# Optimization experiments

Hardware: AMD Instinct MI355X
Metric: run time of the kernel (lower is better)

Reference implementation:

```python
import jax, jax.numpy as jnp
import numpy as np

N, E = 100000, 1600000
NF, HC, NC = 32, 64, 64


def setup_inputs() -> dict:
    key = jax.random.key(0)
    ks = jax.random.split(key, 12)
    s = 0.05
    return {
        "x": jax.random.normal(ks[0], (N, NF), dtype=jnp.float32),
        "edge_index": jax.random.randint(ks[1], (2, E), 0, N, dtype=jnp.int64),
        "eps1": jnp.float32(0.0),
        "eps2": jnp.float32(0.0),
        "W1a": jax.random.normal(ks[2], (NF, HC), dtype=jnp.float32) * s,
        "b1a": jnp.zeros((HC,), dtype=jnp.float32),
        "W1b": jax.random.normal(ks[3], (HC, HC), dtype=jnp.float32) * s,
        "b1b": jnp.zeros((HC,), dtype=jnp.float32),
        "W2a": jax.random.normal(ks[4], (HC, HC), dtype=jnp.float32) * s,
        "b2a": jnp.zeros((HC,), dtype=jnp.float32),
        "W2b": jax.random.normal(ks[5], (HC, NC), dtype=jnp.float32) * s,
        "b2b": jnp.zeros((NC,), dtype=jnp.float32),
    }


def _gin_conv(h, src, dst, eps, Wa, ba, Wb, bb, num_nodes):
    # sum-aggregate neighbor features: out[dst] += h[src]
    agg = jax.ops.segment_sum(h[src], dst, num_segments=num_nodes)
    z = (1.0 + eps) * h + agg
    # 2-layer MLP: Linear -> ReLU -> Linear
    z = jax.nn.relu(z @ Wa + ba)
    return z @ Wb + bb


def reference(x, edge_index, eps1, eps2, W1a, b1a, W1b, b1b, W2a, b2a, W2b, b2b):
    src, dst = edge_index[0], edge_index[1]
    n = x.shape[0]
    emb = _gin_conv(x, src, dst, eps1, W1a, b1a, W1b, b1b, n)  # [N, HC]
    h = jax.nn.relu(emb)  # dropout is identity in eval mode
    logits = _gin_conv(h, src, dst, eps2, W2a, b2a, W2b, b2b, n)  # [N, NC]
    return (logits, emb)
```

## Files before the change

kernel.cpp:

```cpp
#include <hip/hip_runtime.h>


#define NFEAT 32
#define HID   64
#define NCLS  64

#define BSH   9
#define BNODES 512
#define NBKT_MAX 256
#define BCAP  16384
#define ECAP  2048

typedef unsigned int uint;
typedef unsigned short ushortT;
typedef __attribute__((ext_vector_type(8))) short bf16x8;
typedef __attribute__((ext_vector_type(4))) float f32x4;

__device__ __forceinline__ int clampi(int v, int hi){ v = v < 0 ? 0 : v; return v > hi ? hi : v; }

__device__ __forceinline__ ushortT f2b(float f){
  uint u = __float_as_uint(f);
  u = (u + 0x7FFFu + ((u >> 16) & 1u)) >> 16;
  return (ushortT)u;
}
__device__ __forceinline__ float b2f_lo(uint u){ return __uint_as_float(u << 16); }
__device__ __forceinline__ float b2f_hi(uint u){ return __uint_as_float(u & 0xFFFF0000u); }
__device__ __forceinline__ uint pack2(float lo, float hi){
  return (uint)f2b(lo) | ((uint)f2b(hi) << 16);
}


__global__ void k_prep(const float* __restrict__ x, ushortT* __restrict__ xb, int n4,
                       const float* __restrict__ W1a, const float* __restrict__ W1b,
                       const float* __restrict__ W2a, const float* __restrict__ W2b,
                       ushortT* __restrict__ T1a, ushortT* __restrict__ T1b,
                       ushortT* __restrict__ T2a, ushortT* __restrict__ T2b,
                       int* __restrict__ bktCnt, int nbkt){
  int t = blockIdx.x*256 + threadIdx.x;
  if (t < n4){
    float4 v = reinterpret_cast<const float4*>(x)[t];
    ushort4 o = { f2b(v.x), f2b(v.y), f2b(v.z), f2b(v.w) };
    reinterpret_cast<ushort4*>(xb)[t] = o;
  }
  if (t < nbkt) bktCnt[t] = 0;
  if (t < 14336){
    const float* W; ushortT* T; int K; int base;
    if      (t <  2048){ W=W1a; T=T1a; K=32; base=0;     }
    else if (t <  6144){ W=W1b; T=T1b; K=64; base=2048;  }
    else if (t < 10240){ W=W2a; T=T2a; K=64; base=6144;  }
    else               { W=W2b; T=T2b; K=64; base=10240; }
    int o = t - base;
    int k = o >> 6, c = o & 63;
    T[c*K + k] = f2b(W[o]);
  }
}


__global__ void k_bucket(const int* __restrict__ src, const int* __restrict__ dst,
                         int E, int N, int nbkt,
                         int* __restrict__ bktCnt, int* __restrict__ bktData){
  __shared__ int s_cnt[NBKT_MAX];
  __shared__ int s_base[NBKT_MAX];
  const int t = threadIdx.x;
  for (int j = t; j < nbkt; j += 256) s_cnt[j] = 0;
  __syncthreads();

  const int e0 = blockIdx.x * 4096;
  const int e1 = min(e0 + 4096, E);
  for (int e = e0 + t; e < e1; e += 256){
    int d = clampi(dst[e], N-1);
    atomicAdd(&s_cnt[d >> BSH], 1);
  }
  __syncthreads();
  for (int j = t; j < nbkt; j += 256){
    int c = s_cnt[j];
    s_base[j] = (c > 0) ? atomicAdd(&bktCnt[j], c) : 0;
    s_cnt[j] = 0;
  }
  __syncthreads();
  for (int e = e0 + t; e < e1; e += 256){
    int d = clampi(dst[e], N-1);
    int s = clampi(src[e], N-1);
    int b = d >> BSH;
    int p = s_base[b] + atomicAdd(&s_cnt[b], 1);
    if (p < BCAP)
      bktData[(size_t)b * BCAP + p] = ((d & (BNODES-1)) << 17) | s;
  }
}


__global__ void k_bktscan(const int* __restrict__ bktCnt, int nbkt,
                          int* __restrict__ bktBase, int* __restrict__ rowptr, int N){
  __shared__ int s[NBKT_MAX];
  const int t = threadIdx.x;
  int v = (t < nbkt) ? min(bktCnt[t], BCAP) : 0;
  s[t] = v;
  __syncthreads();
  for (int off = 1; off < NBKT_MAX; off <<= 1){
    int add = (t >= off) ? s[t-off] : 0;
    __syncthreads();
    s[t] += add;
    __syncthreads();
  }
  if (t < nbkt) bktBase[t] = s[t] - v;
  if (t == nbkt-1){ bktBase[nbkt] = s[t]; rowptr[N] = s[t]; }
}


__global__ __launch_bounds__(BNODES)
void k_build(const int* __restrict__ bktCnt, const int* __restrict__ bktBase,
             const int* __restrict__ bktData,
             int* __restrict__ rowptr, int* __restrict__ eidx, int N){
  __shared__ int s_h[BNODES];
  __shared__ int s_cur[BNODES];
  const int b = blockIdx.x, t = threadIdx.x;
  const int cnt  = min(bktCnt[b], BCAP);
  const int base = bktBase[b];
  const int* __restrict__ data = bktData + (size_t)b * BCAP;

  s_h[t] = 0;
  __syncthreads();
  for (int e = t; e < cnt; e += BNODES) atomicAdd(&s_h[data[e] >> 17], 1);
  __syncthreads();

  int deg = s_h[t];
  for (int off = 1; off < BNODES; off <<= 1){
    int add = (t >= off) ? s_h[t-off] : 0;
    __syncthreads();
    s_h[t] += add;
    __syncthreads();
  }
  int excl = s_h[t] - deg;
  int node = b * BNODES + t;
  if (node < N) rowptr[node] = base + excl;
  s_cur[t] = excl;
  __syncthreads();

  for (int e = t; e < cnt; e += BNODES){
    int val = data[e];
    int d = val >> 17;
    int p = atomicAdd(&s_cur[d], 1);
    eidx[base + p] = val & 0x1FFFF;
  }
}


template<int K, bool WRITE_HB>
__global__ __launch_bounds__(512)
void k_fused(const uint4* __restrict__ f4,
             const int* __restrict__ rowptr, const int* __restrict__ eidx,
             const float* __restrict__ epsP,
             const ushortT* __restrict__ WaT,
             const float* __restrict__ ba,
             const ushortT* __restrict__ WbT,
             const float* __restrict__ bb,
             float* __restrict__ out,
             ushortT* __restrict__ hb, int N){
  constexpr int RS = K/8;
  constexpr int CH = RS/4;
  constexpr int U  = (CH == 1) ? 4 : 2;
  __shared__ int s_row[65];
  __shared__ int s_eidx[ECAP];
  __shared__ __align__(16) ushortT zt[64*K];
  __shared__ __align__(16) ushortT ht[64*64];
  const int t = threadIdx.x;
  const int row0 = blockIdx.x * 64;

  const int e0 = rowptr[min(row0, N)];
  const int e1 = rowptr[min(row0 + 64, N)];
  if (t < 65){
    int idx = row0 + t; if (idx > N) idx = N;
    s_row[t] = rowptr[idx];
  }
  const int cnt = e1 - e0;
  for (int j = t; j < cnt && j < ECAP; j += 512) s_eidx[j] = eidx[e0 + j];
  __syncthreads();

  {
    const int n = t >> 3;
    const int L = t & 7;
    const int q = L & 3;
    const int s = L >> 2;
    const int node = row0 + n;
    float acc[CH*8];
    #pragma unroll
    for (int j = 0; j < CH*8; ++j) acc[j] = 0.f;

    const int b = s_row[n] - e0;
    const int e = s_row[n+1] - e0;
    int i = b + s;
    for (; i + 2*(U-1) < e; i += 2*U){
      int src[U];
      #pragma unroll
      for (int u = 0; u < U; ++u){
        int ii = i + 2*u;
        src[u] = (ii < ECAP) ? s_eidx[ii] : eidx[e0 + ii];
      }
      uint4 v[U][CH];
      #pragma unroll
      for (int u = 0; u < U; ++u)
        #pragma unroll
        for (int c = 0; c < CH; ++c)
          v[u][c] = f4[(size_t)src[u]*RS + q*CH + c];
      #pragma unroll
      for (int u = 0; u < U; ++u)
        #pragma unroll
        for (int c = 0; c < CH; ++c){
          acc[c*8+0] += b2f_lo(v[u][c].x); acc[c*8+1] += b2f_hi(v[u][c].x);
          acc[c*8+2] += b2f_lo(v[u][c].y); acc[c*8+3] += b2f_hi(v[u][c].y);
          acc[c*8+4] += b2f_lo(v[u][c].z); acc[c*8+5] += b2f_hi(v[u][c].z);
          acc[c*8+6] += b2f_lo(v[u][c].w); acc[c*8+7] += b2f_hi(v[u][c].w);
        }
    }
    for (; i < e; i += 2){
      int src0 = (i < ECAP) ? s_eidx[i] : eidx[e0 + i];
      #pragma unroll
      for (int c = 0; c < CH; ++c){
        uint4 v = f4[(size_t)src0*RS + q*CH + c];
        acc[c*8+0] += b2f_lo(v.x); acc[c*8+1] += b2f_hi(v.x);
        acc[c*8+2] += b2f_lo(v.y); acc[c*8+3] += b2f_hi(v.y);
        acc[c*8+4] += b2f_lo(v.z); acc[c*8+5] += b2f_hi(v.z);
        acc[c*8+6] += b2f_lo(v.w); acc[c*8+7] += b2f_hi(v.w);
      }
    }
    if (s == 1 && node < N){
      const float se = 1.0f + epsP[0];
      #pragma unroll
      for (int c = 0; c < CH; ++c){
        uint4 v = f4[(size_t)node*RS + q*CH + c];
        acc[c*8+0] = fmaf(se, b2f_lo(v.x), acc[c*8+0]);
        acc[c*8+1] = fmaf(se, b2f_hi(v.x), acc[c*8+1]);
        acc[c*8+2] = fmaf(se, b2f_lo(v.y), acc[c*8+2]);
        acc[c*8+3] = fmaf(se, b2f_hi(v.y), acc[c*8+3]);
        acc[c*8+4] = fmaf(se, b2f_lo(v.z), acc[c*8+4]);
        acc[c*8+5] = fmaf(se, b2f_hi(v.z), acc[c*8+5]);
        acc[c*8+6] = fmaf(se, b2f_lo(v.w), acc[c*8+6]);
        acc[c*8+7] = fmaf(se, b2f_hi(v.w), acc[c*8+7]);
      }
    }
    #pragma unroll
    for (int j = 0; j < CH*8; ++j) acc[j] += __shfl_xor(acc[j], 4);
    if (s == 0){
      #pragma unroll
      for (int c = 0; c < CH; ++c){
        uint4 z;
        z.x = pack2(acc[c*8+0], acc[c*8+1]);
        z.y = pack2(acc[c*8+2], acc[c*8+3]);
        z.z = pack2(acc[c*8+4], acc[c*8+5]);
        z.w = pack2(acc[c*8+6], acc[c*8+7]);
        reinterpret_cast<uint4*>(zt)[n*RS + q*CH + c] = z;
      }
    }
  }
  __syncthreads();

  const int w  = t >> 6;
  const int l  = t & 63;
  const int lr = l & 15;
  const int lg = l >> 4;
  const int rf = w & 3;
  const int c0 = (w >> 2) * 2;
  f32x4 c1[2];
  #pragma unroll
  for (int cl = 0; cl < 2; ++cl){ float bv = ba[(c0+cl)*16 + lr]; c1[cl] = (f32x4){bv,bv,bv,bv}; }
  #pragma unroll
  for (int kf = 0; kf < K/32; ++kf){
    bf16x8 a = *reinterpret_cast<const bf16x8*>(&zt[(rf*16 + lr)*K + kf*32 + lg*8]);
    #pragma unroll
    for (int cl = 0; cl < 2; ++cl){
      bf16x8 bfr = *reinterpret_cast<const bf16x8*>(&WaT[((c0+cl)*16 + lr)*K + kf*32 + lg*8]);
      c1[cl] = __builtin_amdgcn_mfma_f32_16x16x32_bf16(a, bfr, c1[cl], 0, 0, 0);
    }
  }
  #pragma unroll
  for (int cl = 0; cl < 2; ++cl)
    #pragma unroll
    for (int r = 0; r < 4; ++r)
      ht[(rf*16 + lg*4 + r)*64 + (c0+cl)*16 + lr] = f2b(fmaxf(c1[cl][r], 0.f));
  __syncthreads();

  f32x4 c2[2];
  #pragma unroll
  for (int cl = 0; cl < 2; ++cl){ float bv = bb[(c0+cl)*16 + lr]; c2[cl] = (f32x4){bv,bv,bv,bv}; }
  #pragma unroll
  for (int kf = 0; kf < 2; ++kf){
    bf16x8 a = *reinterpret_cast<const bf16x8*>(&ht[(rf*16 + lr)*64 + kf*32 + lg*8]);
    #pragma unroll
    for (int cl = 0; cl < 2; ++cl){
      bf16x8 bfr = *reinterpret_cast<const bf16x8*>(&WbT[((c0+cl)*16 + lr)*64 + kf*32 + lg*8]);
      c2[cl] = __builtin_amdgcn_mfma_f32_16x16x32_bf16(a, bfr, c2[cl], 0, 0, 0);
    }
  }
  #pragma unroll
  for (int cl = 0; cl < 2; ++cl)
    #pragma unroll
    for (int r = 0; r < 4; ++r){
      int row = row0 + rf*16 + lg*4 + r;
      if (row < N){
        float v = c2[cl][r];
        out[(size_t)row*64 + (c0+cl)*16 + lr] = v;
        if (WRITE_HB) hb[(size_t)row*64 + (c0+cl)*16 + lr] = f2b(fmaxf(v, 0.f));
      }
    }
}


extern "C" void kernel_launch(void* const* d_in, const int* in_sizes, int n_in,
                              void* d_out, int out_size, void* d_ws, size_t ws_size,
                              hipStream_t stream) {
  const int N = in_sizes[0] / NFEAT;
  const int E = in_sizes[1] / 2;
  const int nbkt = (N + BNODES - 1) / BNODES;

  const float* x    = (const float*)d_in[0];
  const int*   ei   = (const int*)d_in[1];
  const int*   srcI = ei;
  const int*   dstI = ei + E;
  const float* eps1 = (const float*)d_in[2];
  const float* eps2 = (const float*)d_in[3];
  const float* W1a  = (const float*)d_in[4];
  const float* b1a  = (const float*)d_in[5];
  const float* W1b  = (const float*)d_in[6];
  const float* b1b  = (const float*)d_in[7];
  const float* W2a  = (const float*)d_in[8];
  const float* b2a  = (const float*)d_in[9];
  const float* W2b  = (const float*)d_in[10];
  const float* b2b  = (const float*)d_in[11];

  float* outLogits = (float*)d_out;
  float* outEmb    = outLogits + (size_t)N * HID;

  char* w = (char*)d_ws;
  size_t off = 0;
  auto alloc = [&](size_t bytes) -> void* {
    void* p = w + off;
    off = (off + bytes + 255) & ~(size_t)255;
    return p;
  };
  int*     rowptr  = (int*)alloc((size_t)(N+1) * sizeof(int));
  int*     eidx    = (int*)alloc((size_t)E * sizeof(int));
  int*     bktCnt  = (int*)alloc((size_t)NBKT_MAX * sizeof(int));
  int*     bktBase = (int*)alloc((size_t)(NBKT_MAX+1) * sizeof(int));
  ushortT* T1a     = (ushortT*)alloc(64*32*sizeof(ushortT));
  ushortT* T1b     = (ushortT*)alloc(64*64*sizeof(ushortT));
  ushortT* T2a     = (ushortT*)alloc(64*64*sizeof(ushortT));
  ushortT* T2b     = (ushortT*)alloc(64*64*sizeof(ushortT));
  int*     bktData = (int*)alloc((size_t)NBKT_MAX * BCAP * sizeof(int));
  ushortT* xb      = (ushortT*)alloc((size_t)N * NFEAT * sizeof(ushortT));
  ushortT* hb      = (ushortT*)alloc((size_t)N * HID * sizeof(ushortT));

  const int n4 = N * NFEAT / 4;
  k_prep<<<(n4+255)/256, 256, 0, stream>>>(x, xb, n4, W1a, W1b, W2a, W2b,
                                           T1a, T1b, T2a, T2b, bktCnt, nbkt);

  k_bucket <<<(E+4095)/4096, 256, 0, stream>>>(srcI, dstI, E, N, nbkt, bktCnt, bktData);
  k_bktscan<<<1, NBKT_MAX, 0, stream>>>(bktCnt, nbkt, bktBase, rowptr, N);
  k_build  <<<nbkt, BNODES, 0, stream>>>(bktCnt, bktBase, bktData, rowptr, eidx, N);

  const int nblk = (N + 63) / 64;
  k_fused<NFEAT, true><<<nblk, 512, 0, stream>>>((const uint4*)xb, rowptr, eidx,
      eps1, T1a, b1a, T1b, b1b, outEmb, hb, N);

  k_fused<HID, false><<<nblk, 512, 0, stream>>>((const uint4*)hb, rowptr, eidx,
      eps2, T2a, b2a, T2b, b2b, outLogits, (ushortT*)nullptr, N);
}
```

Before: 125.3 us.

## Fold bucket scan into build, deepen masked gather unroll, pad LDS tiles

Removes the separate single-block scan kernel by having every k_build block redundantly compute the bucket prefix sum in shared memory, saving one launch. The gather loop doubles its unroll factor and replaces the unrolled-loop-plus-scalar-tail structure with a masked FMA loop over shared-memory edge indices, so more loads are in flight per iteration; out-of-range slots still issue loads that are then discarded. The zt and ht staging tiles get padded row strides to reduce LDS bank conflicts in the MFMA operand reads. The deeper unroll raises register pressure, which may cut occupancy.

```diff
diff --git a/kernel.cpp b/kernel.cpp
--- a/kernel.cpp
+++ b/kernel.cpp
@@ -89,33 +89,26 @@
 }
 
 
-__global__ void k_bktscan(const int* __restrict__ bktCnt, int nbkt,
-                          int* __restrict__ bktBase, int* __restrict__ rowptr, int N){
-  __shared__ int s[NBKT_MAX];
-  const int t = threadIdx.x;
-  int v = (t < nbkt) ? min(bktCnt[t], BCAP) : 0;
-  s[t] = v;
-  __syncthreads();
-  for (int off = 1; off < NBKT_MAX; off <<= 1){
-    int add = (t >= off) ? s[t-off] : 0;
-    __syncthreads();
-    s[t] += add;
-    __syncthreads();
-  }
-  if (t < nbkt) bktBase[t] = s[t] - v;
-  if (t == nbkt-1){ bktBase[nbkt] = s[t]; rowptr[N] = s[t]; }
-}
-
-
 __global__ __launch_bounds__(BNODES)
-void k_build(const int* __restrict__ bktCnt, const int* __restrict__ bktBase,
-             const int* __restrict__ bktData,
-             int* __restrict__ rowptr, int* __restrict__ eidx, int N){
+void k_build(const int* __restrict__ bktCnt, const int* __restrict__ bktData,
+             int nbkt, int* __restrict__ rowptr, int* __restrict__ eidx, int N){
+  __shared__ int s_bs[NBKT_MAX];
   __shared__ int s_h[BNODES];
   __shared__ int s_cur[BNODES];
   const int b = blockIdx.x, t = threadIdx.x;
+
+  if (t < NBKT_MAX) s_bs[t] = (t < nbkt) ? min(bktCnt[t], BCAP) : 0;
+  __syncthreads();
+  for (int off = 1; off < NBKT_MAX; off <<= 1){
+    int add = 0;
+    if (t < NBKT_MAX && t >= off) add = s_bs[t-off];
+    __syncthreads();
+    if (t < NBKT_MAX) s_bs[t] += add;
+    __syncthreads();
+  }
   const int cnt  = min(bktCnt[b], BCAP);
-  const int base = bktBase[b];
+  const int base = s_bs[b] - cnt;
+  if (b == 0 && t == 0) rowptr[N] = s_bs[nbkt-1];
   const int* __restrict__ data = bktData + (size_t)b * BCAP;
 
   s_h[t] = 0;
@@ -158,11 +151,13 @@
              ushortT* __restrict__ hb, int N){
   constexpr int RS = K/8;
   constexpr int CH = RS/4;
-  constexpr int U  = (CH == 1) ? 4 : 2;
+  constexpr int U  = (CH == 1) ? 8 : 4;
+  constexpr int ZS = K + 8;
+  constexpr int HS = 72;
   __shared__ int s_row[65];
   __shared__ int s_eidx[ECAP];
-  __shared__ __align__(16) ushortT zt[64*K];
-  __shared__ __align__(16) ushortT ht[64*64];
+  __shared__ __align__(16) ushortT zt[64*ZS];
+  __shared__ __align__(16) ushortT ht[64*HS];
   const int t = threadIdx.x;
   const int row0 = blockIdx.x * 64;
 
@@ -186,15 +181,16 @@
     #pragma unroll
     for (int j = 0; j < CH*8; ++j) acc[j] = 0.f;
 
-    const int b = s_row[n] - e0;
-    const int e = s_row[n+1] - e0;
-    int i = b + s;
-    for (; i + 2*(U-1) < e; i += 2*U){
-      int src[U];
+    const int b    = s_row[n] - e0;
+    const int e    = s_row[n+1] - e0;
+    const int iend = min(e, ECAP);
+    for (int i = b + s; i < iend; i += 2*U){
+      float m[U]; int src[U];
       #pragma unroll
       for (int u = 0; u < U; ++u){
         int ii = i + 2*u;
-        src[u] = (ii < ECAP) ? s_eidx[ii] : eidx[e0 + ii];
+        m[u]   = (ii < iend) ? 1.f : 0.f;
+        src[u] = s_eidx[min(ii, iend-1)];
       }
       uint4 v[U][CH];
       #pragma unroll
@@ -206,21 +202,29 @@
       for (int u = 0; u < U; ++u)
         #pragma unroll
         for (int c = 0; c < CH; ++c){
-          acc[c*8+0] += b2f_lo(v[u][c].x); acc[c*8+1] += b2f_hi(v[u][c].x);
-          acc[c*8+2] += b2f_lo(v[u][c].y); acc[c*8+3] += b2f_hi(v[u][c].y);
-          acc[c*8+4] += b2f_lo(v[u][c].z); acc[c*8+5] += b2f_hi(v[u][c].z);
-          acc[c*8+6] += b2f_lo(v[u][c].w); acc[c*8+7] += b2f_hi(v[u][c].w);
+          acc[c*8+0] = fmaf(m[u], b2f_lo(v[u][c].x), acc[c*8+0]);
+          acc[c*8+1] = fmaf(m[u], b2f_hi(v[u][c].x), acc[c*8+1]);
+          acc[c*8+2] = fmaf(m[u], b2f_lo(v[u][c].y), acc[c*8+2]);
+          acc[c*8+3] = fmaf(m[u], b2f_hi(v[u][c].y), acc[c*8+3]);
+          acc[c*8+4] = fmaf(m[u], b2f_lo(v[u][c].z), acc[c*8+4]);
+          acc[c*8+5] = fmaf(m[u], b2f_hi(v[u][c].z), acc[c*8+5]);
+          acc[c*8+6] = fmaf(m[u], b2f_lo(v[u][c].w), acc[c*8+6]);
+          acc[c*8+7] = fmaf(m[u], b2f_hi(v[u][c].w), acc[c*8+7]);
         }
     }
-    for (; i < e; i += 2){
-      int src0 = (i < ECAP) ? s_eidx[i] : eidx[e0 + i];
-      #pragma unroll
-      for (int c = 0; c < CH; ++c){
-        uint4 v = f4[(size_t)src0*RS + q*CH + c];
-        acc[c*8+0] += b2f_lo(v.x); acc[c*8+1] += b2f_hi(v.x);
-        acc[c*8+2] += b2f_lo(v.y); acc[c*8+3] += b2f_hi(v.y);
-        acc[c*8+4] += b2f_lo(v.z); acc[c*8+5] += b2f_hi(v.z);
-        acc[c*8+6] += b2f_lo(v.w); acc[c*8+7] += b2f_hi(v.w);
+    {
+      int rem = iend - (b + s);
+      int i2  = (rem > 0) ? (b + s + ((rem + 1) & ~1)) : (b + s);
+      for (; i2 < e; i2 += 2){
+        int src0 = eidx[e0 + i2];
+        #pragma unroll
+        for (int c = 0; c < CH; ++c){
+          uint4 v = f4[(size_t)src0*RS + q*CH + c];
+          acc[c*8+0] += b2f_lo(v.x); acc[c*8+1] += b2f_hi(v.x);
+          acc[c*8+2] += b2f_lo(v.y); acc[c*8+3] += b2f_hi(v.y);
+          acc[c*8+4] += b2f_lo(v.z); acc[c*8+5] += b2f_hi(v.z);
+          acc[c*8+6] += b2f_lo(v.w); acc[c*8+7] += b2f_hi(v.w);
+        }
       }
     }
     if (s == 1 && node < N){
@@ -248,7 +252,7 @@
         z.y = pack2(acc[c*8+2], acc[c*8+3]);
         z.z = pack2(acc[c*8+4], acc[c*8+5]);
         z.w = pack2(acc[c*8+6], acc[c*8+7]);
-        reinterpret_cast<uint4*>(zt)[n*RS + q*CH + c] = z;
+        *reinterpret_cast<uint4*>(&zt[n*ZS + (q*CH + c)*8]) = z;
       }
     }
   }
@@ -265,7 +269,7 @@
   for (int cl = 0; cl < 2; ++cl){ float bv = ba[(c0+cl)*16 + lr]; c1[cl] = (f32x4){bv,bv,bv,bv}; }
   #pragma unroll
   for (int kf = 0; kf < K/32; ++kf){
-    bf16x8 a = *reinterpret_cast<const bf16x8*>(&zt[(rf*16 + lr)*K + kf*32 + lg*8]);
+    bf16x8 a = *reinterpret_cast<const bf16x8*>(&zt[(rf*16 + lr)*ZS + kf*32 + lg*8]);
     #pragma unroll
     for (int cl = 0; cl < 2; ++cl){
       bf16x8 bfr = *reinterpret_cast<const bf16x8*>(&WaT[((c0+cl)*16 + lr)*K + kf*32 + lg*8]);
@@ -276,7 +280,7 @@
   for (int cl = 0; cl < 2; ++cl)
     #pragma unroll
     for (int r = 0; r < 4; ++r)
-      ht[(rf*16 + lg*4 + r)*64 + (c0+cl)*16 + lr] = f2b(fmaxf(c1[cl][r], 0.f));
+      ht[(rf*16 + lg*4 + r)*HS + (c0+cl)*16 + lr] = f2b(fmaxf(c1[cl][r], 0.f));
   __syncthreads();
 
   f32x4 c2[2];
@@ -284,7 +288,7 @@
   for (int cl = 0; cl < 2; ++cl){ float bv = bb[(c0+cl)*16 + lr]; c2[cl] = (f32x4){bv,bv,bv,bv}; }
   #pragma unroll
   for (int kf = 0; kf < 2; ++kf){
-    bf16x8 a = *reinterpret_cast<const bf16x8*>(&ht[(rf*16 + lr)*64 + kf*32 + lg*8]);
+    bf16x8 a = *reinterpret_cast<const bf16x8*>(&ht[(rf*16 + lr)*HS + kf*32 + lg*8]);
     #pragma unroll
     for (int cl = 0; cl < 2; ++cl){
       bf16x8 bfr = *reinterpret_cast<const bf16x8*>(&WbT[((c0+cl)*16 + lr)*64 + kf*32 + lg*8]);
@@ -340,7 +344,6 @@
   int*     rowptr  = (int*)alloc((size_t)(N+1) * sizeof(int));
   int*     eidx    = (int*)alloc((size_t)E * sizeof(int));
   int*     bktCnt  = (int*)alloc((size_t)NBKT_MAX * sizeof(int));
-  int*     bktBase = (int*)alloc((size_t)(NBKT_MAX+1) * sizeof(int));
   ushortT* T1a     = (ushortT*)alloc(64*32*sizeof(ushortT));
   ushortT* T1b     = (ushortT*)alloc(64*64*sizeof(ushortT));
   ushortT* T2a     = (ushortT*)alloc(64*64*sizeof(ushortT));
@@ -353,9 +356,8 @@
   k_prep<<<(n4+255)/256, 256, 0, stream>>>(x, xb, n4, W1a, W1b, W2a, W2b,
                                            T1a, T1b, T2a, T2b, bktCnt, nbkt);
 
-  k_bucket <<<(E+4095)/4096, 256, 0, stream>>>(srcI, dstI, E, N, nbkt, bktCnt, bktData);
-  k_bktscan<<<1, NBKT_MAX, 0, stream>>>(bktCnt, nbkt, bktBase, rowptr, N);
-  k_build  <<<nbkt, BNODES, 0, stream>>>(bktCnt, bktBase, bktData, rowptr, eidx, N);
+  k_bucket<<<(E+4095)/4096, 256, 0, stream>>>(srcI, dstI, E, N, nbkt, bktCnt, bktData);
+  k_build <<<nbkt, BNODES, 0, stream>>>(bktCnt, bktData, nbkt, rowptr, eidx, N);
 
   const int nblk = (N + 63) / 64;
   k_fused<NFEAT, true><<<nblk, 512, 0, stream>>>((const uint4*)xb, rowptr, eidx,
```

Measured after the change: 133.2 us. +6.4%, slower.
